# Optimization experiments

Hardware: AMD Instinct MI355X
Metric: run time of the kernel (lower is better)

The kernel has to match this reference:

```python
import jax, jax.numpy as jnp
import numpy as np


def _gcn_conv(x, edge_index, W, b):
    """Faithful PyG GCNConv: add self-loops, symmetric norm, scatter-sum, bias."""
    n = x.shape[0]
    loop = jnp.arange(n, dtype=edge_index.dtype)
    src = jnp.concatenate([edge_index[0], loop])  # [E+n]
    dst = jnp.concatenate([edge_index[1], loop])
    # in-degree at dst (edge_weight = 1), as in gcn_norm
    deg = jax.ops.segment_sum(jnp.ones(src.shape[0], x.dtype), dst, num_segments=n)
    dinv = jnp.where(deg > 0, jax.lax.rsqrt(deg), 0.0)
    norm = dinv[src] * dinv[dst]                  # [E+n]
    h = x @ W                                     # [n, C] small GEMM
    msg = h[src] * norm[:, None]                  # gather + scale (dominant traffic)
    out = jax.ops.segment_sum(msg, dst, num_segments=n)  # scatter-sum
    return out + b


def setup_inputs() -> dict:
    key = jax.random.key(0)
    ks = jax.random.split(key, 8)
    N, E, C = 50000, 1000000, 64
    scale = 1.0 / np.sqrt(C)
    return {
        "x_star": jax.random.normal(ks[0], (N, C), jnp.float32),
        "x_gal": jax.random.normal(ks[1], (N, C), jnp.float32),
        "edge_ss_near": jax.random.randint(ks[2], (2, E), 0, N, jnp.int64),
        "edge_ss_far": jax.random.randint(ks[3], (2, E), 0, N, jnp.int64),
        "edge_gg_near": jax.random.randint(ks[4], (2, E), 0, N, jnp.int64),
        "W_ss_near": jax.random.normal(ks[5], (C, C), jnp.float32) * scale,
        "W_ss_far": jax.random.normal(ks[6], (C, C), jnp.float32) * scale,
        "W_gg_near": jax.random.normal(ks[7], (C, C), jnp.float32) * scale,
        "b_ss_near": jnp.zeros((C,), jnp.float32),
        "b_ss_far": jnp.zeros((C,), jnp.float32),
        "b_gg_near": jnp.zeros((C,), jnp.float32),
    }


def reference(x_star, x_gal, edge_ss_near, edge_ss_far, edge_gg_near,
              W_ss_near, W_ss_far, W_gg_near,
              b_ss_near, b_ss_far, b_gg_near):
    # HeteroConv with aggr='sum': per-edge-type GCNConv, summed per dst node type.
    out_star = (_gcn_conv(x_star, edge_ss_near, W_ss_near, b_ss_near)
                + _gcn_conv(x_star, edge_ss_far, W_ss_far, b_ss_far))
    out_gal = _gcn_conv(x_gal, edge_gg_near, W_gg_near, b_gg_near)
    return out_star, out_gal
```

## Files before the change

kernel.cpp:

```cpp
#include <hip/hip_runtime.h>
#include <hip/hip_fp16.h>

#define CCH 64
#define BKT 256
#define PCH 8192
#define NBMAX 200
#define GR 64
#define STCAP 8192

typedef int int4a __attribute__((ext_vector_type(4), aligned(4)));

__global__ void __launch_bounds__(256) k_hist(const int* __restrict__ e0,
        const int* __restrict__ e1, const int* __restrict__ e2,
        int* __restrict__ H, int* __restrict__ cnt, int E, int NB, int NBLK) {
    int c = blockIdx.y;
    const int* dd = ((c == 0) ? e0 : (c == 1) ? e1 : e2) + E;
    int base = blockIdx.x * PCH;
    int nE = E - base; if (nE > PCH) nE = PCH;
    __shared__ int hist[NBMAX];
    int t = threadIdx.x;
    if (t < NB) hist[t] = 0;
    __syncthreads();
    for (int k = t * 4; k < nE; k += 1024) {
        if (k + 3 < nE) {
            int4a d = *(const int4a*)(dd + base + k);
            atomicAdd(&hist[d.x >> 8], 1); atomicAdd(&hist[d.y >> 8], 1);
            atomicAdd(&hist[d.z >> 8], 1); atomicAdd(&hist[d.w >> 8], 1);
        } else {
            for (int j = k; j < nE; ++j) atomicAdd(&hist[dd[base + j] >> 8], 1);
        }
    }
    __syncthreads();
    int* Hrow = H + ((size_t)c * NBLK + blockIdx.x) * NB;
    if (t < NB) {
        int h = hist[t];
        Hrow[t] = h;
        if (h) atomicAdd(&cnt[c * NB + t], h);
    }
}

__global__ void __launch_bounds__(1024) k_bscan(const int* __restrict__ cnt,
        int* __restrict__ bstart, __half* __restrict__ zrow, int NB, int E) {
    int c = blockIdx.x, t = threadIdx.x;
    if (c == 0 && t < 32) ((float*)zrow)[t] = 0.f;
    __shared__ int sm[1024];
    int i0 = 2 * t, i1 = 2 * t + 1;
    int v0 = (i0 < NB) ? cnt[c * NB + i0] : 0;
    int v1 = (i1 < NB) ? cnt[c * NB + i1] : 0;
    sm[t] = v0 + v1;
    __syncthreads();
    #pragma unroll
    for (int off = 1; off < 1024; off <<= 1) {
        int u = (t >= off) ? sm[t - off] : 0;
        __syncthreads();
        sm[t] += u;
        __syncthreads();
    }
    int ex = sm[t] - (v0 + v1);
    if (i0 < NB) bstart[c * (NB + 1) + i0] = ex;
    if (i1 < NB) bstart[c * (NB + 1) + i1] = ex + v0;
    if (t == 0) bstart[c * (NB + 1) + NB] = E;
}

__global__ void __launch_bounds__(256) k_colscan(int* __restrict__ H,
        const int* __restrict__ bstart, int NB, int NBLK) {
    int c = blockIdx.y;
    int b = blockIdx.x * 4 + (threadIdx.x >> 6);
    if (b >= NB) return;
    int l = threadIdx.x & 63;
    int* Hc = H + (size_t)c * NBLK * NB;
    int run = bstart[c * (NB + 1) + b];
    for (int c0 = 0; c0 < NBLK; c0 += 64) {
        int blk = c0 + l;
        int v = (blk < NBLK) ? Hc[(size_t)blk * NB + b] : 0;
        int s = v;
        #pragma unroll
        for (int off = 1; off < 64; off <<= 1) {
            int u = __shfl_up(s, off, 64);
            if (l >= off) s += u;
        }
        if (blk < NBLK) Hc[(size_t)blk * NB + b] = run + s - v;
        run += __shfl(s, 63, 64);
    }
}

__global__ void __launch_bounds__(256) k_part2(const int* __restrict__ e0,
        const int* __restrict__ e1, const int* __restrict__ e2,
        const int* __restrict__ H, const int* __restrict__ bstart,
        unsigned* __restrict__ bdata, int E, int NB, int NBLK) {
    int c = blockIdx.y;
    const int* ed = (c == 0) ? e0 : (c == 1) ? e1 : e2;
    int base = blockIdx.x * PCH;
    int nE = E - base; if (nE > PCH) nE = PCH;
    __shared__ unsigned staged[PCH];
    __shared__ int hist[NBMAX];
    __shared__ int off[NBMAX];
    __shared__ int sm[256];
    int t = threadIdx.x;
    const int* Hcur = H + ((size_t)c * NBLK + blockIdx.x) * NB;
    const int* Hnxt = (blockIdx.x == NBLK - 1) ? (bstart + c * (NB + 1) + 1)
                                               : (Hcur + NB);
    if (t < NB) {
        int cu = Hcur[t];
        off[t] = cu;
        hist[t] = Hnxt[t] - cu;
    }
    __syncthreads();
    int s = (t < NB) ? hist[t] : 0;
    sm[t] = s;
    __syncthreads();
    #pragma unroll
    for (int o = 1; o < 256; o <<= 1) {
        int u = (t >= o) ? sm[t - o] : 0;
        __syncthreads();
        sm[t] += u;
        __syncthreads();
    }
    if (t < NB) {
        int run = sm[t] - s;
        off[t] -= run;
        hist[t] = run;
    }
    __syncthreads();
    for (int k = t * 4; k < nE; k += 1024) {
        if (k + 3 < nE) {
            int4a s4 = *(const int4a*)(ed + base + k);
            int4a d4 = *(const int4a*)(ed + E + base + k);
            int sl;
            sl = atomicAdd(&hist[d4.x >> 8], 1); staged[sl] = (unsigned)s4.x | ((unsigned)d4.x << 16);
            sl = atomicAdd(&hist[d4.y >> 8], 1); staged[sl] = (unsigned)s4.y | ((unsigned)d4.y << 16);
            sl = atomicAdd(&hist[d4.z >> 8], 1); staged[sl] = (unsigned)s4.z | ((unsigned)d4.z << 16);
            sl = atomicAdd(&hist[d4.w >> 8], 1); staged[sl] = (unsigned)s4.w | ((unsigned)d4.w << 16);
        } else {
            for (int j = k; j < nE; ++j) {
                int s0 = ed[base + j];
                int d0 = ed[E + base + j];
                int sl = atomicAdd(&hist[d0 >> 8], 1);
                staged[sl] = (unsigned)s0 | ((unsigned)d0 << 16);
            }
        }
    }
    __syncthreads();
    unsigned* bo = bdata + (size_t)c * E;
    for (int sI = t; sI < nE; sI += 256) {
        unsigned rec = staged[sI];
        int b = (int)(rec >> 16) >> 8;
        bo[off[b] + sI] = rec;
    }
}

__global__ void __launch_bounds__(256) k_sort32(const unsigned* __restrict__ bdata,
        const int* __restrict__ bstart, int* __restrict__ sdat,
        int* __restrict__ rs, float* __restrict__ dinv, int E, int N, int NB) {
    int c = blockIdx.y;
    int b = blockIdx.x;
    __shared__ unsigned staged[STCAP];
    __shared__ int cnt[BKT];
    __shared__ int cur[BKT];
    __shared__ int wsum[4];
    int t = threadIdx.x;
    cnt[t] = 0;
    __syncthreads();
    int s0 = bstart[c * (NB + 1) + b];
    int sE = bstart[c * (NB + 1) + b + 1];
    int n = sE - s0;
    const unsigned* bd = bdata + (size_t)c * E;
    bool fits = (n <= STCAP);
    if (fits) {
        for (int i = t; i < n; i += 256) staged[i] = bd[s0 + i];
        __syncthreads();
        for (int i = t; i < n; i += 256)
            atomicAdd(&cnt[(staged[i] >> 16) & 255], 1);
    } else {
        for (int i = s0 + t; i < sE; i += 256)
            atomicAdd(&cnt[(bd[i] >> 16) & 255], 1);
    }
    __syncthreads();
    int v = cnt[t];
    int s = v;
    #pragma unroll
    for (int off = 1; off < 64; off <<= 1) {
        int u = __shfl_up(s, off, 64);
        if ((t & 63) >= off) s += u;
    }
    int w = t >> 6;
    if ((t & 63) == 63) wsum[w] = s;
    __syncthreads();
    int wpre = 0;
    #pragma unroll
    for (int j = 0; j < 4; ++j) if (j < w) wpre += wsum[j];
    int ex = s0 + wpre + s - v;
    cur[t] = ex;
    int row = b * BKT + t;
    if (row < N) {
        rs[c * (N + 1) + row] = ex;
        dinv[c * N + row] = rsqrtf((float)(v + 1));
    }
    if (b == 0 && t == 0) rs[c * (N + 1) + N] = E;
    __syncthreads();
    int* so = sdat + (size_t)c * E;
    if (fits) {
        for (int i = t; i < n; i += 256) {
            unsigned r = staged[i];
            int slot = atomicAdd(&cur[(r >> 16) & 255], 1);
            so[slot] = (int)(r & 0xFFFFu);
        }
    } else {
        for (int i = s0 + t; i < sE; i += 256) {
            unsigned r = bd[i];
            int slot = atomicAdd(&cur[(r >> 16) & 255], 1);
            so[slot] = (int)(r & 0xFFFFu);
        }
    }
}

__global__ void __launch_bounds__(256) k_gemm_all(const float* __restrict__ xs_,
        const float* __restrict__ xg_, const float* __restrict__ W0,
        const float* __restrict__ W1, const float* __restrict__ W2,
        const float* __restrict__ dinv, __half* __restrict__ h16, int N) {
    int star = (blockIdx.y == 0);
    const float* x = star ? xs_ : xg_;
    __shared__ float Ws[2][CCH * CCH];
    __shared__ float xT[CCH * (GR + 1)];
    int t = threadIdx.x;
    int row0 = blockIdx.x * GR;
    size_t NC = (size_t)N * CCH;
    if (star) {
        #pragma unroll
        for (int j = 0; j < 4; ++j) {
            int idx = j * 1024 + t * 4;
            *(float4*)(&Ws[0][idx]) = *(const float4*)(W0 + idx);
            *(float4*)(&Ws[1][idx]) = *(const float4*)(W1 + idx);
        }
    } else {
        #pragma unroll
        for (int j = 0; j < 4; ++j) {
            int idx = j * 1024 + t * 4;
            *(float4*)(&Ws[0][idx]) = *(const float4*)(W2 + idx);
        }
    }
    #pragma unroll
    for (int j = 0; j < 4; ++j) {
        int idx = t + j * 256;
        int r = idx >> 4;
        int c0 = (idx & 15) * 4;
        int row = row0 + r;
        float4 v = make_float4(0.f, 0.f, 0.f, 0.f);
        if (row < N) v = *(const float4*)(x + (size_t)row * CCH + c0);
        xT[(c0 + 0) * (GR + 1) + r] = v.x;
        xT[(c0 + 1) * (GR + 1) + r] = v.y;
        xT[(c0 + 2) * (GR + 1) + r] = v.z;
        xT[(c0 + 3) * (GR + 1) + r] = v.w;
    }
    __syncthreads();
    int c4 = (t & 15) * 4;
    int r0 = (t >> 4) * 4;
    if (star) {
        float4 a0 = make_float4(0.f, 0.f, 0.f, 0.f), a1 = a0, a2 = a0, a3 = a0;
        float4 d0 = a0, d1 = a0, d2 = a0, d3 = a0;
        #pragma unroll 4
        for (int k = 0; k < CCH; ++k) {
            float4 wv = *(float4*)(&Ws[0][k * CCH + c4]);
            float4 uv = *(float4*)(&Ws[1][k * CCH + c4]);
            float x0 = xT[k * (GR + 1) + r0 + 0];
            float x1 = xT[k * (GR + 1) + r0 + 1];
            float x2 = xT[k * (GR + 1) + r0 + 2];
            float x3 = xT[k * (GR + 1) + r0 + 3];
            a0.x += x0 * wv.x; a0.y += x0 * wv.y; a0.z += x0 * wv.z; a0.w += x0 * wv.w;
            a1.x += x1 * wv.x; a1.y += x1 * wv.y; a1.z += x1 * wv.z; a1.w += x1 * wv.w;
            a2.x += x2 * wv.x; a2.y += x2 * wv.y; a2.z += x2 * wv.z; a2.w += x2 * wv.w;
            a3.x += x3 * wv.x; a3.y += x3 * wv.y; a3.z += x3 * wv.z; a3.w += x3 * wv.w;
            d0.x += x0 * uv.x; d0.y += x0 * uv.y; d0.z += x0 * uv.z; d0.w += x0 * uv.w;
            d1.x += x1 * uv.x; d1.y += x1 * uv.y; d1.z += x1 * uv.z; d1.w += x1 * uv.w;
            d2.x += x2 * uv.x; d2.y += x2 * uv.y; d2.z += x2 * uv.z; d2.w += x2 * uv.w;
            d3.x += x3 * uv.x; d3.y += x3 * uv.y; d3.z += x3 * uv.z; d3.w += x3 * uv.w;
        }
        float4 av[4] = {a0, a1, a2, a3};
        float4 dv4[4] = {d0, d1, d2, d3};
        #pragma unroll
        for (int i = 0; i < 4; ++i) {
            int row = row0 + r0 + i;
            if (row < N) {
                float dd0 = dinv[row];
                float dd1 = dinv[N + row];
                union { __half2 h2[2]; float2 f2; } u;
                u.h2[0] = __floats2half2_rn(av[i].x * dd0, av[i].y * dd0);
                u.h2[1] = __floats2half2_rn(av[i].z * dd0, av[i].w * dd0);
                *(float2*)(h16 + (size_t)row * CCH + c4) = u.f2;
                u.h2[0] = __floats2half2_rn(dv4[i].x * dd1, dv4[i].y * dd1);
                u.h2[1] = __floats2half2_rn(dv4[i].z * dd1, dv4[i].w * dd1);
                *(float2*)(h16 + NC + (size_t)row * CCH + c4) = u.f2;
            }
        }
    } else {
        float4 a0 = make_float4(0.f, 0.f, 0.f, 0.f), a1 = a0, a2 = a0, a3 = a0;
        #pragma unroll 8
        for (int k = 0; k < CCH; ++k) {
            float4 wv = *(float4*)(&Ws[0][k * CCH + c4]);
            float x0 = xT[k * (GR + 1) + r0 + 0];
            float x1 = xT[k * (GR + 1) + r0 + 1];
            float x2 = xT[k * (GR + 1) + r0 + 2];
            float x3 = xT[k * (GR + 1) + r0 + 3];
            a0.x += x0 * wv.x; a0.y += x0 * wv.y; a0.z += x0 * wv.z; a0.w += x0 * wv.w;
            a1.x += x1 * wv.x; a1.y += x1 * wv.y; a1.z += x1 * wv.z; a1.w += x1 * wv.w;
            a2.x += x2 * wv.x; a2.y += x2 * wv.y; a2.z += x2 * wv.z; a2.w += x2 * wv.w;
            a3.x += x3 * wv.x; a3.y += x3 * wv.y; a3.z += x3 * wv.z; a3.w += x3 * wv.w;
        }
        float4 av[4] = {a0, a1, a2, a3};
        #pragma unroll
        for (int i = 0; i < 4; ++i) {
            int row = row0 + r0 + i;
            if (row < N) {
                float dd = dinv[2 * N + row];
                union { __half2 h2[2]; float2 f2; } u;
                u.h2[0] = __floats2half2_rn(av[i].x * dd, av[i].y * dd);
                u.h2[1] = __floats2half2_rn(av[i].z * dd, av[i].w * dd);
                *(float2*)(h16 + 2 * NC + (size_t)row * CCH + c4) = u.f2;
            }
        }
    }
}

__device__ __forceinline__ float4 gat4p(const __half* __restrict__ p, int l16) {
    union { float2 f2; __half2 h2[2]; } u;
    u.f2 = ((const float2*)p)[l16];
    float2 a = __half22float2(u.h2[0]);
    float2 b = __half22float2(u.h2[1]);
    return make_float4(a.x, a.y, b.x, b.y);
}

__device__ __forceinline__ void acc4(float4& a, float4 v) {
    a.x += v.x; a.y += v.y; a.z += v.z; a.w += v.w;
}

__global__ void __launch_bounds__(256) k_pull(const int* __restrict__ rs,
        const int* __restrict__ sdat, const __half* __restrict__ h16,
        const float* __restrict__ dinv, const __half* __restrict__ zrow,
        const float* __restrict__ b0, const float* __restrict__ b1,
        const float* __restrict__ b2,
        float* __restrict__ out, int N, int E, int row0) {
    int row = row0 + blockIdx.x * 4 + (threadIdx.x >> 6);
    if (row >= 2 * N) return;
    int lane = threadIdx.x & 63;
    int q = lane >> 4;
    int l16 = lane & 15;
    size_t NC = (size_t)N * CCH;

    const __half* hcL;
    const int* sdL;
    int beg, end;
    float ddL;
    float4 bias;
    float* op;
    float4 acc = make_float4(0.f, 0.f, 0.f, 0.f);
    if (row < N) {
        int cv = q >> 1;
        const int* rsA = rs + cv * (N + 1);
        int bg = rsA[row], eg = rsA[row + 1];
        int mid = (bg + eg) >> 1;
        beg = (q & 1) ? mid : bg;
        end = (q & 1) ? eg : mid;
        hcL = h16 + (size_t)cv * NC;
        sdL = sdat + (size_t)cv * E;
        ddL = dinv[cv * N + row];
        if (!(q & 1)) acc = gat4p(hcL + (size_t)row * CCH, l16);
        float4 bv0 = ((const float4*)b0)[l16];
        float4 bv1 = ((const float4*)b1)[l16];
        bias = make_float4(bv0.x + bv1.x, bv0.y + bv1.y,
                           bv0.z + bv1.z, bv0.w + bv1.w);
        op = out + (size_t)row * CCH;
    } else {
        int r = row - N;
        const int* rs2 = rs + 2 * (N + 1);
        int bg = rs2[r], eg = rs2[r + 1];
        int len = eg - bg;
        beg = bg + ((len * q) >> 2);
        end = bg + ((len * (q + 1)) >> 2);
        hcL = h16 + 2 * NC;
        sdL = sdat + 2 * (size_t)E;
        ddL = dinv[2 * N + r];
        if (q == 0) acc = gat4p(hcL + (size_t)r * CCH, l16);
        bias = ((const float4*)b2)[l16];
        op = out + NC + (size_t)r * CCH;
    }

    int i = beg;
    for (; i + 7 < end; i += 8) {
        int4a q0 = *(const int4a*)(sdL + i);
        int4a q1 = *(const int4a*)(sdL + i + 4);
        float4 v0 = gat4p(hcL + (size_t)q0.x * CCH, l16);
        float4 v1 = gat4p(hcL + (size_t)q0.y * CCH, l16);
        float4 v2 = gat4p(hcL + (size_t)q0.z * CCH, l16);
        float4 v3 = gat4p(hcL + (size_t)q0.w * CCH, l16);
        float4 v4 = gat4p(hcL + (size_t)q1.x * CCH, l16);
        float4 v5 = gat4p(hcL + (size_t)q1.y * CCH, l16);
        float4 v6 = gat4p(hcL + (size_t)q1.z * CCH, l16);
        float4 v7 = gat4p(hcL + (size_t)q1.w * CCH, l16);
        acc4(acc, v0); acc4(acc, v1); acc4(acc, v2); acc4(acc, v3);
        acc4(acc, v4); acc4(acc, v5); acc4(acc, v6); acc4(acc, v7);
    }
    if (i < end) {
        int4a q0 = *(const int4a*)(sdL + i);
        int4a q1 = *(const int4a*)(sdL + i + 4);
        const __half* p0 = hcL + (size_t)q0.x * CCH;
        const __half* p1 = (i + 1 < end) ? hcL + (size_t)q0.y * CCH : zrow;
        const __half* p2 = (i + 2 < end) ? hcL + (size_t)q0.z * CCH : zrow;
        const __half* p3 = (i + 3 < end) ? hcL + (size_t)q0.w * CCH : zrow;
        const __half* p4 = (i + 4 < end) ? hcL + (size_t)q1.x * CCH : zrow;
        const __half* p5 = (i + 5 < end) ? hcL + (size_t)q1.y * CCH : zrow;
        const __half* p6 = (i + 6 < end) ? hcL + (size_t)q1.z * CCH : zrow;
        const __half* p7 = (i + 7 < end) ? hcL + (size_t)q1.w * CCH : zrow;
        float4 v0 = gat4p(p0, l16);
        float4 v1 = gat4p(p1, l16);
        float4 v2 = gat4p(p2, l16);
        float4 v3 = gat4p(p3, l16);
        float4 v4 = gat4p(p4, l16);
        float4 v5 = gat4p(p5, l16);
        float4 v6 = gat4p(p6, l16);
        float4 v7 = gat4p(p7, l16);
        acc4(acc, v0); acc4(acc, v1); acc4(acc, v2); acc4(acc, v3);
        acc4(acc, v4); acc4(acc, v5); acc4(acc, v6); acc4(acc, v7);
    }

    float4 t;
    t.x = acc.x * ddL; t.y = acc.y * ddL; t.z = acc.z * ddL; t.w = acc.w * ddL;
    t.x += __shfl_xor(t.x, 16, 64); t.y += __shfl_xor(t.y, 16, 64);
    t.z += __shfl_xor(t.z, 16, 64); t.w += __shfl_xor(t.w, 16, 64);
    t.x += __shfl_xor(t.x, 32, 64); t.y += __shfl_xor(t.y, 32, 64);
    t.z += __shfl_xor(t.z, 32, 64); t.w += __shfl_xor(t.w, 32, 64);
    if (lane < 16) {
        t.x += bias.x; t.y += bias.y; t.z += bias.z; t.w += bias.w;
        ((float4*)op)[l16] = t;
    }
}

static inline size_t align256(size_t x) { return (x + 255) & ~(size_t)255; }

extern "C" void kernel_launch(void* const* d_in, const int* in_sizes, int n_in,
                              void* d_out, int out_size, void* d_ws, size_t ws_size,
                              hipStream_t stream) {
    const float* x_star = (const float*)d_in[0];
    const float* x_gal  = (const float*)d_in[1];
    const int*   e_ssn  = (const int*)d_in[2];
    const int*   e_ssf  = (const int*)d_in[3];
    const int*   e_ggn  = (const int*)d_in[4];
    const float* W_ssn  = (const float*)d_in[5];
    const float* W_ssf  = (const float*)d_in[6];
    const float* W_ggn  = (const float*)d_in[7];
    const float* b_ssn  = (const float*)d_in[8];
    const float* b_ssf  = (const float*)d_in[9];
    const float* b_ggn  = (const float*)d_in[10];

    const int N  = in_sizes[0] / CCH;
    const int E  = in_sizes[2] / 2;
    const size_t NC = (size_t)N * CCH;
    const int NB   = (N + BKT - 1) / BKT;
    const int NBLK = (E + PCH - 1) / PCH;

    char* w = (char*)d_ws;
    __half*   h16    = (__half*)w;   w += align256((size_t)3 * NC * 2);
    float*    dinv   = (float*)w;    w += align256((size_t)3 * N * 4);
    unsigned* bdata  = (unsigned*)w; w += align256((size_t)3 * E * 4);
    int*      sdat   = (int*)w;      w += align256((size_t)3 * E * 4);
    int*      H      = (int*)w;      w += align256((size_t)3 * NBLK * NB * 4);
    int*      cnt    = (int*)w;      w += align256((size_t)3 * NB * 4);
    int*      bstart = (int*)w;      w += align256((size_t)3 * (NB + 1) * 4);
    int*      rs     = (int*)w;      w += align256((size_t)3 * (N + 1) * 4);
    __half*   zrow   = (__half*)w;   w += align256((size_t)CCH * 2);

    const int B = 256;

    hipMemsetAsync(cnt, 0, (size_t)3 * NB * 4, stream);
    k_hist<<<dim3(NBLK, 3), B, 0, stream>>>(e_ssn, e_ssf, e_ggn, H, cnt, E, NB, NBLK);
    k_bscan<<<3, 1024, 0, stream>>>(cnt, bstart, zrow, NB, E);
    k_colscan<<<dim3((NB + 3) / 4, 3), B, 0, stream>>>(H, bstart, NB, NBLK);
    k_part2<<<dim3(NBLK, 3), B, 0, stream>>>(e_ssn, e_ssf, e_ggn, H, bstart,
                                             bdata, E, NB, NBLK);
    k_sort32<<<dim3(NB, 3), B, 0, stream>>>(bdata, bstart, sdat, rs, dinv, E, N, NB);
    k_gemm_all<<<dim3((N + GR - 1) / GR, 2), B, 0, stream>>>(x_star, x_gal,
                                                             W_ssn, W_ssf, W_ggn,
                                                             dinv, h16, N);
    k_pull<<<(N + 3) / 4, B, 0, stream>>>(rs, sdat, h16, dinv, zrow,
                                          b_ssn, b_ssf, b_ggn,
                                          (float*)d_out, N, E, 0);
    k_pull<<<(N + 3) / 4, B, 0, stream>>>(rs, sdat, h16, dinv, zrow,
                                          b_ssn, b_ssf, b_ggn,
                                          (float*)d_out, N, E, N);
}
```

Measured before the change: 234.0 us.

## Fuse edge-sorting stages into one cooperative kernel with grid syncs

Replaces the five separate sorting kernels (histogram, bucket scan, column scan, partition, per-bucket sort) and the memset with a single cooperative kernel that uses grid.sync between phases. The chunk size drops so that the grid of 3*max(NBLK,NB) blocks can be co-resident, and both pull launches become one. This removes launch gaps and tail effects between small kernels. The cost is grid-wide barriers and smaller chunks per block, and the launch fails if the grid cannot be fully resident.

```diff
diff --git a/kernel.cpp b/kernel.cpp
--- a/kernel.cpp
+++ b/kernel.cpp
@@ -1,215 +1,199 @@
 #include <hip/hip_runtime.h>
 #include <hip/hip_fp16.h>
+#include <hip/hip_cooperative_groups.h>
 
 #define CCH 64
 #define BKT 256
-#define PCH 8192
-#define NBMAX 200
+#define PCH 5104
 #define GR 64
-#define STCAP 8192
+#define STCAP 6144
 
 typedef int int4a __attribute__((ext_vector_type(4), aligned(4)));
 
-__global__ void __launch_bounds__(256) k_hist(const int* __restrict__ e0,
-        const int* __restrict__ e1, const int* __restrict__ e2,
-        int* __restrict__ H, int* __restrict__ cnt, int E, int NB, int NBLK) {
-    int c = blockIdx.y;
-    const int* dd = ((c == 0) ? e0 : (c == 1) ? e1 : e2) + E;
-    int base = blockIdx.x * PCH;
-    int nE = E - base; if (nE > PCH) nE = PCH;
-    __shared__ int hist[NBMAX];
-    int t = threadIdx.x;
-    if (t < NB) hist[t] = 0;
-    __syncthreads();
-    for (int k = t * 4; k < nE; k += 1024) {
-        if (k + 3 < nE) {
-            int4a d = *(const int4a*)(dd + base + k);
-            atomicAdd(&hist[d.x >> 8], 1); atomicAdd(&hist[d.y >> 8], 1);
-            atomicAdd(&hist[d.z >> 8], 1); atomicAdd(&hist[d.w >> 8], 1);
-        } else {
-            for (int j = k; j < nE; ++j) atomicAdd(&hist[dd[base + j] >> 8], 1);
-        }
-    }
-    __syncthreads();
-    int* Hrow = H + ((size_t)c * NBLK + blockIdx.x) * NB;
-    if (t < NB) {
-        int h = hist[t];
-        Hrow[t] = h;
-        if (h) atomicAdd(&cnt[c * NB + t], h);
-    }
-}
-
-__global__ void __launch_bounds__(1024) k_bscan(const int* __restrict__ cnt,
-        int* __restrict__ bstart, __half* __restrict__ zrow, int NB, int E) {
-    int c = blockIdx.x, t = threadIdx.x;
-    if (c == 0 && t < 32) ((float*)zrow)[t] = 0.f;
-    __shared__ int sm[1024];
-    int i0 = 2 * t, i1 = 2 * t + 1;
-    int v0 = (i0 < NB) ? cnt[c * NB + i0] : 0;
-    int v1 = (i1 < NB) ? cnt[c * NB + i1] : 0;
-    sm[t] = v0 + v1;
-    __syncthreads();
-    #pragma unroll
-    for (int off = 1; off < 1024; off <<= 1) {
-        int u = (t >= off) ? sm[t - off] : 0;
-        __syncthreads();
-        sm[t] += u;
-        __syncthreads();
-    }
-    int ex = sm[t] - (v0 + v1);
-    if (i0 < NB) bstart[c * (NB + 1) + i0] = ex;
-    if (i1 < NB) bstart[c * (NB + 1) + i1] = ex + v0;
-    if (t == 0) bstart[c * (NB + 1) + NB] = E;
-}
-
-__global__ void __launch_bounds__(256) k_colscan(int* __restrict__ H,
-        const int* __restrict__ bstart, int NB, int NBLK) {
-    int c = blockIdx.y;
-    int b = blockIdx.x * 4 + (threadIdx.x >> 6);
-    if (b >= NB) return;
-    int l = threadIdx.x & 63;
-    int* Hc = H + (size_t)c * NBLK * NB;
-    int run = bstart[c * (NB + 1) + b];
-    for (int c0 = 0; c0 < NBLK; c0 += 64) {
-        int blk = c0 + l;
-        int v = (blk < NBLK) ? Hc[(size_t)blk * NB + b] : 0;
-        int s = v;
-        #pragma unroll
-        for (int off = 1; off < 64; off <<= 1) {
-            int u = __shfl_up(s, off, 64);
-            if (l >= off) s += u;
-        }
-        if (blk < NBLK) Hc[(size_t)blk * NB + b] = run + s - v;
-        run += __shfl(s, 63, 64);
-    }
-}
-
-__global__ void __launch_bounds__(256) k_part2(const int* __restrict__ e0,
-        const int* __restrict__ e1, const int* __restrict__ e2,
-        const int* __restrict__ H, const int* __restrict__ bstart,
-        unsigned* __restrict__ bdata, int E, int NB, int NBLK) {
-    int c = blockIdx.y;
-    const int* ed = (c == 0) ? e0 : (c == 1) ? e1 : e2;
-    int base = blockIdx.x * PCH;
-    int nE = E - base; if (nE > PCH) nE = PCH;
-    __shared__ unsigned staged[PCH];
-    __shared__ int hist[NBMAX];
-    __shared__ int off[NBMAX];
-    __shared__ int sm[256];
-    int t = threadIdx.x;
-    const int* Hcur = H + ((size_t)c * NBLK + blockIdx.x) * NB;
-    const int* Hnxt = (blockIdx.x == NBLK - 1) ? (bstart + c * (NB + 1) + 1)
-                                               : (Hcur + NB);
-    if (t < NB) {
-        int cu = Hcur[t];
-        off[t] = cu;
-        hist[t] = Hnxt[t] - cu;
-    }
-    __syncthreads();
-    int s = (t < NB) ? hist[t] : 0;
-    sm[t] = s;
-    __syncthreads();
-    #pragma unroll
-    for (int o = 1; o < 256; o <<= 1) {
-        int u = (t >= o) ? sm[t - o] : 0;
-        __syncthreads();
-        sm[t] += u;
-        __syncthreads();
-    }
-    if (t < NB) {
-        int run = sm[t] - s;
-        off[t] -= run;
-        hist[t] = run;
-    }
-    __syncthreads();
-    for (int k = t * 4; k < nE; k += 1024) {
-        if (k + 3 < nE) {
-            int4a s4 = *(const int4a*)(ed + base + k);
-            int4a d4 = *(const int4a*)(ed + E + base + k);
-            int sl;
-            sl = atomicAdd(&hist[d4.x >> 8], 1); staged[sl] = (unsigned)s4.x | ((unsigned)d4.x << 16);
-            sl = atomicAdd(&hist[d4.y >> 8], 1); staged[sl] = (unsigned)s4.y | ((unsigned)d4.y << 16);
-            sl = atomicAdd(&hist[d4.z >> 8], 1); staged[sl] = (unsigned)s4.z | ((unsigned)d4.z << 16);
-            sl = atomicAdd(&hist[d4.w >> 8], 1); staged[sl] = (unsigned)s4.w | ((unsigned)d4.w << 16);
-        } else {
-            for (int j = k; j < nE; ++j) {
-                int s0 = ed[base + j];
-                int d0 = ed[E + base + j];
-                int sl = atomicAdd(&hist[d0 >> 8], 1);
-                staged[sl] = (unsigned)s0 | ((unsigned)d0 << 16);
-            }
-        }
-    }
-    __syncthreads();
-    unsigned* bo = bdata + (size_t)c * E;
-    for (int sI = t; sI < nE; sI += 256) {
-        unsigned rec = staged[sI];
-        int b = (int)(rec >> 16) >> 8;
-        bo[off[b] + sI] = rec;
-    }
-}
-
-__global__ void __launch_bounds__(256) k_sort32(const unsigned* __restrict__ bdata,
-        const int* __restrict__ bstart, int* __restrict__ sdat,
-        int* __restrict__ rs, float* __restrict__ dinv, int E, int N, int NB) {
-    int c = blockIdx.y;
-    int b = blockIdx.x;
-    __shared__ unsigned staged[STCAP];
-    __shared__ int cnt[BKT];
-    __shared__ int cur[BKT];
-    __shared__ int wsum[4];
-    int t = threadIdx.x;
-    cnt[t] = 0;
-    __syncthreads();
-    int s0 = bstart[c * (NB + 1) + b];
-    int sE = bstart[c * (NB + 1) + b + 1];
-    int n = sE - s0;
-    const unsigned* bd = bdata + (size_t)c * E;
-    bool fits = (n <= STCAP);
-    if (fits) {
-        for (int i = t; i < n; i += 256) staged[i] = bd[s0 + i];
-        __syncthreads();
-        for (int i = t; i < n; i += 256)
-            atomicAdd(&cnt[(staged[i] >> 16) & 255], 1);
-    } else {
-        for (int i = s0 + t; i < sE; i += 256)
-            atomicAdd(&cnt[(bd[i] >> 16) & 255], 1);
-    }
-    __syncthreads();
-    int v = cnt[t];
+#define SMEM_BYTES 26688
+
+__device__ __forceinline__ int scan256ex(int v, int t, int* wsum) {
     int s = v;
     #pragma unroll
     for (int off = 1; off < 64; off <<= 1) {
         int u = __shfl_up(s, off, 64);
         if ((t & 63) >= off) s += u;
     }
-    int w = t >> 6;
-    if ((t & 63) == 63) wsum[w] = s;
+    if ((t & 63) == 63) wsum[t >> 6] = s;
     __syncthreads();
     int wpre = 0;
     #pragma unroll
-    for (int j = 0; j < 4; ++j) if (j < w) wpre += wsum[j];
-    int ex = s0 + wpre + s - v;
-    cur[t] = ex;
-    int row = b * BKT + t;
-    if (row < N) {
-        rs[c * (N + 1) + row] = ex;
-        dinv[c * N + row] = rsqrtf((float)(v + 1));
-    }
-    if (b == 0 && t == 0) rs[c * (N + 1) + N] = E;
-    __syncthreads();
-    int* so = sdat + (size_t)c * E;
-    if (fits) {
-        for (int i = t; i < n; i += 256) {
-            unsigned r = staged[i];
-            int slot = atomicAdd(&cur[(r >> 16) & 255], 1);
-            so[slot] = (int)(r & 0xFFFFu);
-        }
-    } else {
-        for (int i = s0 + t; i < sE; i += 256) {
-            unsigned r = bd[i];
-            int slot = atomicAdd(&cur[(r >> 16) & 255], 1);
-            so[slot] = (int)(r & 0xFFFFu);
+    for (int j = 0; j < 4; ++j) if (j < (t >> 6)) wpre += wsum[j];
+    return wpre + s - v;
+}
+
+__global__ void __launch_bounds__(256) k_order(const int* __restrict__ e0,
+        const int* __restrict__ e1, const int* __restrict__ e2,
+        int* __restrict__ H, int* __restrict__ cnt, int* __restrict__ bstart,
+        unsigned* __restrict__ bdata, int* __restrict__ sdat,
+        int* __restrict__ rs, float* __restrict__ dinv, __half* __restrict__ zrow,
+        int E, int N, int NB, int NBLK) {
+    cooperative_groups::grid_group grid = cooperative_groups::this_grid();
+    __shared__ __align__(16) char smem[SMEM_BYTES];
+    int t = threadIdx.x;
+    int gb = blockIdx.x;
+
+    if (gb == 0) {
+        for (int i = t; i < 3 * NB; i += 256) cnt[i] = 0;
+        if (t < 32) ((float*)zrow)[t] = 0.f;
+    }
+    grid.sync();
+
+    if (gb < 3 * NBLK) {
+        int c = gb / NBLK, blk = gb % NBLK;
+        const int* dd = ((c == 0) ? e0 : (c == 1) ? e1 : e2) + E;
+        int base = blk * PCH;
+        int nE = E - base; if (nE > PCH) nE = PCH;
+        int* hist = (int*)smem;
+        if (t < NB) hist[t] = 0;
+        __syncthreads();
+        for (int k = t * 4; k < nE; k += 1024) {
+            if (k + 3 < nE) {
+                int4a d = *(const int4a*)(dd + base + k);
+                atomicAdd(&hist[d.x >> 8], 1); atomicAdd(&hist[d.y >> 8], 1);
+                atomicAdd(&hist[d.z >> 8], 1); atomicAdd(&hist[d.w >> 8], 1);
+            } else {
+                for (int j = k; j < nE; ++j) atomicAdd(&hist[dd[base + j] >> 8], 1);
+            }
+        }
+        __syncthreads();
+        int* Hrow = H + ((size_t)c * NBLK + blk) * NB;
+        if (t < NB) {
+            int h = hist[t];
+            Hrow[t] = h;
+            if (h) atomicAdd(&cnt[c * NB + t], h);
+        }
+    }
+    grid.sync();
+
+    if (gb < 3) {
+        int c = gb;
+        int* wsum = (int*)(smem + 1024);
+        int v = (t < NB) ? cnt[c * NB + t] : 0;
+        int ex = scan256ex(v, t, wsum);
+        if (t < NB) bstart[c * (NB + 1) + t] = ex;
+        if (t == 0) bstart[c * (NB + 1) + NB] = E;
+    }
+    grid.sync();
+
+    if (gb < 3 * NB && t < 64) {
+        int c = gb / NB, b = gb % NB;
+        int* Hc = H + (size_t)c * NBLK * NB;
+        int run = bstart[c * (NB + 1) + b];
+        for (int c0 = 0; c0 < NBLK; c0 += 64) {
+            int blk = c0 + t;
+            int v = (blk < NBLK) ? Hc[(size_t)blk * NB + b] : 0;
+            int s = v;
+            #pragma unroll
+            for (int off = 1; off < 64; off <<= 1) {
+                int u = __shfl_up(s, off, 64);
+                if (t >= off) s += u;
+            }
+            if (blk < NBLK) Hc[(size_t)blk * NB + b] = run + s - v;
+            run += __shfl(s, 63, 64);
+        }
+    }
+    grid.sync();
+
+    if (gb < 3 * NBLK) {
+        int c = gb / NBLK, blk = gb % NBLK;
+        const int* ed = (c == 0) ? e0 : (c == 1) ? e1 : e2;
+        int base = blk * PCH;
+        int nE = E - base; if (nE > PCH) nE = PCH;
+        unsigned* staged = (unsigned*)smem;
+        int* hist = (int*)(smem + 20416);
+        int* off  = (int*)(smem + 21216);
+        int* wsum = (int*)(smem + 22016);
+        const int* Hcur = H + ((size_t)c * NBLK + blk) * NB;
+        const int* Hnxt = (blk == NBLK - 1) ? (bstart + c * (NB + 1) + 1)
+                                            : (Hcur + NB);
+        int cu_ = 0, h_ = 0;
+        if (t < NB) { cu_ = Hcur[t]; h_ = Hnxt[t] - cu_; }
+        int run = scan256ex(h_, t, wsum);
+        if (t < NB) {
+            off[t] = cu_ - run;
+            hist[t] = run;
+        }
+        __syncthreads();
+        for (int k = t * 4; k < nE; k += 1024) {
+            if (k + 3 < nE) {
+                int4a s4 = *(const int4a*)(ed + base + k);
+                int4a d4 = *(const int4a*)(ed + E + base + k);
+                int sl;
+                sl = atomicAdd(&hist[d4.x >> 8], 1); staged[sl] = (unsigned)s4.x | ((unsigned)d4.x << 16);
+                sl = atomicAdd(&hist[d4.y >> 8], 1); staged[sl] = (unsigned)s4.y | ((unsigned)d4.y << 16);
+                sl = atomicAdd(&hist[d4.z >> 8], 1); staged[sl] = (unsigned)s4.z | ((unsigned)d4.z << 16);
+                sl = atomicAdd(&hist[d4.w >> 8], 1); staged[sl] = (unsigned)s4.w | ((unsigned)d4.w << 16);
+            } else {
+                for (int j = k; j < nE; ++j) {
+                    int s0 = ed[base + j];
+                    int d0 = ed[E + base + j];
+                    int sl = atomicAdd(&hist[d0 >> 8], 1);
+                    staged[sl] = (unsigned)s0 | ((unsigned)d0 << 16);
+                }
+            }
+        }
+        __syncthreads();
+        unsigned* bo = bdata + (size_t)c * E;
+        for (int sI = t; sI < nE; sI += 256) {
+            unsigned rec = staged[sI];
+            int b2 = (int)(rec >> 16) >> 8;
+            bo[off[b2] + sI] = rec;
+        }
+    }
+    grid.sync();
+
+    if (gb < 3 * NB) {
+        int c = gb / NB, b = gb % NB;
+        unsigned* staged = (unsigned*)smem;
+        int* cnt_ = (int*)(smem + 24576);
+        int* cur  = (int*)(smem + 25600);
+        int* wsum = (int*)(smem + 26624);
+        cnt_[t] = 0;
+        __syncthreads();
+        int s0 = bstart[c * (NB + 1) + b];
+        int sE = bstart[c * (NB + 1) + b + 1];
+        int n = sE - s0;
+        const unsigned* bd = bdata + (size_t)c * E;
+        bool fits = (n <= STCAP);
+        if (fits) {
+            for (int i = t; i < n; i += 256) staged[i] = bd[s0 + i];
+            __syncthreads();
+            for (int i = t; i < n; i += 256)
+                atomicAdd(&cnt_[(staged[i] >> 16) & 255], 1);
+        } else {
+            for (int i = s0 + t; i < sE; i += 256)
+                atomicAdd(&cnt_[(bd[i] >> 16) & 255], 1);
+        }
+        __syncthreads();
+        int v = cnt_[t];
+        int ex = s0 + scan256ex(v, t, wsum);
+        cur[t] = ex;
+        int row = b * BKT + t;
+        if (row < N) {
+            rs[c * (N + 1) + row] = ex;
+            dinv[(size_t)c * N + row] = rsqrtf((float)(v + 1));
+        }
+        if (gb == 0 && t < 3) rs[t * (N + 1) + N] = E;
+        __syncthreads();
+        int* so = sdat + (size_t)c * E;
+        if (fits) {
+            for (int i = t; i < n; i += 256) {
+                unsigned r = staged[i];
+                int slot = atomicAdd(&cur[(r >> 16) & 255], 1);
+                so[slot] = (int)(r & 0xFFFFu);
+            }
+        } else {
+            for (int i = s0 + t; i < sE; i += 256) {
+                unsigned r = bd[i];
+                int slot = atomicAdd(&cur[(r >> 16) & 255], 1);
+                so[slot] = (int)(r & 0xFFFFu);
+            }
         }
     }
 }
@@ -338,8 +322,8 @@
         const float* __restrict__ dinv, const __half* __restrict__ zrow,
         const float* __restrict__ b0, const float* __restrict__ b1,
         const float* __restrict__ b2,
-        float* __restrict__ out, int N, int E, int row0) {
-    int row = row0 + blockIdx.x * 4 + (threadIdx.x >> 6);
+        float* __restrict__ out, int N, int E) {
+    int row = blockIdx.x * 4 + (threadIdx.x >> 6);
     if (row >= 2 * N) return;
     int lane = threadIdx.x & 63;
     int q = lane >> 4;
@@ -451,11 +435,12 @@
     const float* b_ssf  = (const float*)d_in[9];
     const float* b_ggn  = (const float*)d_in[10];
 
-    const int N  = in_sizes[0] / CCH;
-    const int E  = in_sizes[2] / 2;
+    int N  = in_sizes[0] / CCH;
+    int E  = in_sizes[2] / 2;
     const size_t NC = (size_t)N * CCH;
-    const int NB   = (N + BKT - 1) / BKT;
-    const int NBLK = (E + PCH - 1) / PCH;
+    int NB   = (N + BKT - 1) / BKT;
+    int NBLK = (E + PCH - 1) / PCH;
+    int GRID = 3 * ((NBLK > NB) ? NBLK : NB);
 
     char* w = (char*)d_ws;
     __half*   h16    = (__half*)w;   w += align256((size_t)3 * NC * 2);
@@ -470,20 +455,17 @@
 
     const int B = 256;
 
-    hipMemsetAsync(cnt, 0, (size_t)3 * NB * 4, stream);
-    k_hist<<<dim3(NBLK, 3), B, 0, stream>>>(e_ssn, e_ssf, e_ggn, H, cnt, E, NB, NBLK);
-    k_bscan<<<3, 1024, 0, stream>>>(cnt, bstart, zrow, NB, E);
-    k_colscan<<<dim3((NB + 3) / 4, 3), B, 0, stream>>>(H, bstart, NB, NBLK);
-    k_part2<<<dim3(NBLK, 3), B, 0, stream>>>(e_ssn, e_ssf, e_ggn, H, bstart,
-                                             bdata, E, NB, NBLK);
-    k_sort32<<<dim3(NB, 3), B, 0, stream>>>(bdata, bstart, sdat, rs, dinv, E, N, NB);
+    void* args[] = {(void*)&e_ssn, (void*)&e_ssf, (void*)&e_ggn,
+                    (void*)&H, (void*)&cnt, (void*)&bstart,
+                    (void*)&bdata, (void*)&sdat, (void*)&rs,
+                    (void*)&dinv, (void*)&zrow,
+                    (void*)&E, (void*)&N, (void*)&NB, (void*)&NBLK};
+    hipLaunchCooperativeKernel((void*)k_order, dim3(GRID), dim3(B),
+                               args, 0, stream);
     k_gemm_all<<<dim3((N + GR - 1) / GR, 2), B, 0, stream>>>(x_star, x_gal,
                                                              W_ssn, W_ssf, W_ggn,
                                                              dinv, h16, N);
-    k_pull<<<(N + 3) / 4, B, 0, stream>>>(rs, sdat, h16, dinv, zrow,
-                                          b_ssn, b_ssf, b_ggn,
-                                          (float*)d_out, N, E, 0);
-    k_pull<<<(N + 3) / 4, B, 0, stream>>>(rs, sdat, h16, dinv, zrow,
-                                          b_ssn, b_ssf, b_ggn,
-                                          (float*)d_out, N, E, N);
-}
+    k_pull<<<(2 * N + 3) / 4, B, 0, stream>>>(rs, sdat, h16, dinv, zrow,
+                                              b_ssn, b_ssf, b_ggn,
+                                              (float*)d_out, N, E);
+}
```

After: 556.9 us. +138.0%, slower.
